# Optimization experiments

Hardware: AMD Instinct MI355X
Metric: run time of the kernel (lower is better)

The kernel has to match this reference:

```python
import jax, jax.numpy as jnp
import numpy as np

EMBED_DIM = 768
NUM_HEADS = 12
HEAD_DIM = EMBED_DIM // NUM_HEADS  # 64
SCALE = HEAD_DIM ** -0.5
B, S = 32, 512


def setup_inputs() -> dict:
    key = jax.random.key(0)
    ks = jax.random.split(key, 10)
    std = EMBED_DIM ** -0.5
    hidden_states = jax.random.normal(ks[0], (B, S, EMBED_DIM), dtype=jnp.float32)
    # causal mask: 0 on/below diagonal, large negative above
    neg = jnp.full((S, S), -1e9, dtype=jnp.float32)
    causal_attention_mask = jnp.broadcast_to(
        jnp.triu(neg, k=1)[None, None, :, :], (B, 1, S, S)
    ).astype(jnp.float32)
    Wq = jax.random.normal(ks[1], (EMBED_DIM, EMBED_DIM), dtype=jnp.float32) * std
    bq = jnp.zeros((EMBED_DIM,), dtype=jnp.float32)
    Wk = jax.random.normal(ks[2], (EMBED_DIM, EMBED_DIM), dtype=jnp.float32) * std
    bk = jnp.zeros((EMBED_DIM,), dtype=jnp.float32)
    Wv = jax.random.normal(ks[3], (EMBED_DIM, EMBED_DIM), dtype=jnp.float32) * std
    bv = jnp.zeros((EMBED_DIM,), dtype=jnp.float32)
    Wo = jax.random.normal(ks[4], (EMBED_DIM, EMBED_DIM), dtype=jnp.float32) * std
    bo = jnp.zeros((EMBED_DIM,), dtype=jnp.float32)
    return {
        "hidden_states": hidden_states,
        "causal_attention_mask": causal_attention_mask,
        "Wq": Wq, "bq": bq, "Wk": Wk, "bk": bk,
        "Wv": Wv, "bv": bv, "Wo": Wo, "bo": bo,
    }


def reference(hidden_states, causal_attention_mask, Wq, bq, Wk, bk, Wv, bv, Wo, bo):
    b, s, e = hidden_states.shape
    # projections; query scaled as in original
    q = (hidden_states @ Wq + bq) * SCALE          # [b,s,e]
    k = hidden_states @ Wk + bk
    v = hidden_states @ Wv + bv
    # [b,h,s,d]
    q = q.reshape(b, s, NUM_HEADS, HEAD_DIM).transpose(0, 2, 1, 3)
    k = k.reshape(b, s, NUM_HEADS, HEAD_DIM).transpose(0, 2, 1, 3)
    v = v.reshape(b, s, NUM_HEADS, HEAD_DIM).transpose(0, 2, 1, 3)
    scores = jnp.einsum("bhqd,bhkd->bhqk", q, k) + causal_attention_mask
    attn = jax.nn.softmax(scores, axis=-1)
    out = jnp.einsum("bhqk,bhkd->bhqd", attn, v)   # [b,h,s,d]
    out = out.transpose(0, 2, 1, 3).reshape(b, s, e)
    return out @ Wo + bo
```

## Files before the change

### kernel.cpp

```cpp
#include <hip/hip_runtime.h>
#include <hip/hip_bf16.h>

typedef __attribute__((ext_vector_type(8))) short bf16x8;
typedef __attribute__((ext_vector_type(4))) float f32x4;
typedef unsigned short u16;
typedef unsigned int u32;

#define MFMA16(a,b,c) __builtin_amdgcn_mfma_f32_16x16x32_bf16((a),(b),(c),0,0,0)
#define FENCE() asm volatile("" ::: "memory")
#define BARRIER() do { FENCE(); __builtin_amdgcn_s_barrier(); FENCE(); } while (0)
#define WAITV(N) asm volatile("s_waitcnt vmcnt(" #N ")" ::: "memory")

__device__ __forceinline__ u16 f2bf(float f) {
  union { float f; u32 u; } c; c.f = f;
  u32 u = c.u;
  return (u16)((u + 0x7FFFu + ((u >> 16) & 1u)) >> 16);
}

__device__ __forceinline__ u32 pk2(float lo, float hi) {
  __hip_bfloat162 h2 = __float22bfloat162_rn(float2{lo, hi});
  union { __hip_bfloat162 h; u32 u; } c; c.h = h2; return c.u;
}

__device__ __forceinline__ void gl_lds16(const u16* g, u16* l) {
  __builtin_amdgcn_global_load_lds((const __attribute__((address_space(1))) void*)g,
                                   (__attribute__((address_space(3))) void*)l, 16, 0, 0);
}

__global__ __launch_bounds__(256) void prep(const float* __restrict__ X,
                                            u16* __restrict__ Xb,
                                            const float* __restrict__ Wq,
                                            const float* __restrict__ Wk,
                                            const float* __restrict__ Wv,
                                            const float* __restrict__ Wo,
                                            u16* __restrict__ WT) {
  const int blk = blockIdx.x, tid = threadIdx.x;
  if (blk < 6144) {
    int i = (blk * 256 + tid) * 8;
    const float4* p = (const float4*)(X + i);
    float4 a = p[0], b = p[1];
    union { u16 h[8]; uint4 v; } o;
    o.h[0] = f2bf(a.x); o.h[1] = f2bf(a.y); o.h[2] = f2bf(a.z); o.h[3] = f2bf(a.w);
    o.h[4] = f2bf(b.x); o.h[5] = f2bf(b.y); o.h[6] = f2bf(b.z); o.h[7] = f2bf(b.w);
    *(uint4*)(Xb + i) = o.v;
  } else {
    __shared__ float t[32][33];
    const int q = blk - 6144;
    const int w = q / 576, p = q % 576;
    const float* W = (w == 0) ? Wq : (w == 1) ? Wk : (w == 2) ? Wv : Wo;
    u16* D = WT + (size_t)w * 768 * 768;
    const int n0 = (p % 24) * 32, k0 = (p / 24) * 32;
    const int tx = tid & 31, ty = tid >> 5;
#pragma unroll
    for (int i = 0; i < 4; ++i)
      t[ty + i * 8][tx] = W[(size_t)(k0 + ty + i * 8) * 768 + n0 + tx];
    __syncthreads();
#pragma unroll
    for (int i = 0; i < 4; ++i)
      D[(size_t)(n0 + ty + i * 8) * 768 + k0 + tx] = f2bf(t[tx][ty + i * 8]);
  }
}


#define STA(bu, t) do { _Pragma("unroll") for (int s_ = 0; s_ < 2; ++s_) { \
    const int r_ = s_ * 128 + srow; \
    gl_lds16(A + (size_t)(M0 + r_) * 768 + (t) * 64 + ((sg ^ (r_ & 7)) << 3), \
             &As[bu][r_ * 64 + sg * 8]); } } while (0)
#define STB(bu, t) do { \
    gl_lds16(BT + (size_t)(N0 + srow) * 768 + (t) * 64 + ((sg ^ (srow & 7)) << 3), \
             &Bs[bu][srow * 64 + sg * 8]); \
    if (srow < 64) { const int r_ = 128 + srow; \
      gl_lds16(BT + (size_t)(N0 + r_) * 768 + (t) * 64 + ((sg ^ (r_ & 7)) << 3), \
               &Bs[bu][r_ * 64 + sg * 8]); } } while (0)

template <int MODE>
__global__ __launch_bounds__(1024, 4)
void gemmN(const u16* __restrict__ A, const u16* __restrict__ BT,
           const float* __restrict__ b0, const float* __restrict__ b1,
           const float* __restrict__ b2,
           u16* __restrict__ oQ, u16* __restrict__ oK, u16* __restrict__ oV,
           float* __restrict__ oF, int nN) {
  constexpr int NT = 12;
  __shared__ __align__(16) u16 As[2][256 * 64];
  __shared__ __align__(16) u16 Bs[2][192 * 64];
  const int tid = threadIdx.x;
  const int wave = tid >> 6, lane = tid & 63;
  const int lg = lane >> 4, l15 = lane & 15;
  const int wr = wave >> 2, wc = wave & 3;
  const int bi = blockIdx.x;
  const int j = bi >> 3;
  const int M0 = ((bi & 7) * 8 + j / nN) * 256;
  const int N0 = (j % nN) * 192;
  const int srow = tid >> 3, sg = tid & 7;

  f32x4 acc[4][3] = {};

  STA(0, 0); STB(0, 0);

#pragma unroll
  for (int t = 0; t < NT; ++t) {
    WAITV(0);
    BARRIER();
    if (t + 1 < NT) { STA((t + 1) & 1, t + 1); STB((t + 1) & 1, t + 1); }
    const int bb = t & 1;
    __builtin_amdgcn_s_setprio(1);
    bf16x8 bfr[3][2];
#pragma unroll
    for (int nt = 0; nt < 3; ++nt)
#pragma unroll
      for (int kh = 0; kh < 2; ++kh) {
        const int row = wc * 48 + nt * 16 + l15;
        bfr[nt][kh] = *(const bf16x8*)&Bs[bb][row * 64 + (((kh * 4 + lg) ^ (row & 7)) << 3)];
      }
#pragma unroll
    for (int mt = 0; mt < 4; ++mt) {
      bf16x8 af[2];
#pragma unroll
      for (int kh = 0; kh < 2; ++kh) {
        const int row = wr * 64 + mt * 16 + l15;
        af[kh] = *(const bf16x8*)&As[bb][row * 64 + (((kh * 4 + lg) ^ (row & 7)) << 3)];
      }
#pragma unroll
      for (int nt = 0; nt < 3; ++nt)
#pragma unroll
        for (int kh = 0; kh < 2; ++kh)
          acc[mt][nt] = MFMA16(af[kh], bfr[nt][kh], acc[mt][nt]);
    }
    __builtin_amdgcn_s_setprio(0);
  }

#pragma unroll
  for (int mt = 0; mt < 4; ++mt) {
    const int r0 = M0 + wr * 64 + mt * 16 + lg * 4;
#pragma unroll
    for (int nt = 0; nt < 3; ++nt) {
      const int ng = N0 + wc * 48 + nt * 16 + l15;
      f32x4 v = acc[mt][nt];
      if (MODE == 1) {
        const float bb = b0[ng];
#pragma unroll
        for (int r = 0; r < 4; ++r)
          oF[(size_t)(r0 + r) * 768 + ng] = v[r] + bb;
      } else {
        const int mat = ng / 768;
        const int col = ng - mat * 768;
        const float bb = (mat == 0 ? b0 : (mat == 1 ? b1 : b2))[col];
        if (mat == 0) {
#pragma unroll
          for (int r = 0; r < 4; ++r)
            oQ[(size_t)(r0 + r) * 768 + col] = f2bf((v[r] + bb) * 0.125f);
        } else if (mat == 1) {
#pragma unroll
          for (int r = 0; r < 4; ++r)
            oK[(size_t)(r0 + r) * 768 + col] = f2bf(v[r] + bb);
        } else {
          const int hh = col >> 6, dd = col & 63;
#pragma unroll
          for (int r = 0; r < 4; ++r) {
            const int rr = r0 + r;
            const int bbx = rr >> 9, ss = rr & 511;
            oV[((size_t)(bbx * 12 + hh) * 64 + dd) * 512 + ss] = f2bf(v[r] + bb);
          }
        }
      }
    }
  }
}

#define STG(bu, kt) do { \
    gl_lds16(Kg0 + (size_t)((kt) * 64 + srow) * 768 + sgr * 8, \
             &Ks[bu][srow * 64 + (tid & 7) * 8]); \
    gl_lds16(Vg0 + (size_t)srow * 512 + (kt) * 64 + sgr * 8, \
             &Vs[bu][srow * 64 + (tid & 7) * 8]); \
  } while (0)

__global__ __launch_bounds__(512, 2)
void flash(const u16* __restrict__ Q, const u16* __restrict__ K,
           const u16* __restrict__ V, u16* __restrict__ O) {
  __shared__ __align__(16) u16 Ks[3][4096];
  __shared__ __align__(16) u16 Vs[3][4096];
  __shared__ __align__(16) u32 Ps[8][16 * 36];
  const int id = blockIdx.x;
  const int qt = id / 384, hb = id % 384;
  const int h = hb % 12, b = hb / 12;
  const int tid = threadIdx.x, wave = tid >> 6, lane = tid & 63;
  const int lg = lane >> 4, l15 = lane & 15;
  const int NT = 2 * qt + 2;
  const int srow = tid >> 3, sgr = (tid & 7) ^ (srow & 7);
  const int qbase = qt * 128 + wave * 16;

  bf16x8 qf[2];
  {
    const u16* qp = Q + (size_t)(b * 512 + qbase + l15) * 768 + h * 64 + lg * 8;
    qf[0] = *(const bf16x8*)qp;
    qf[1] = *(const bf16x8*)(qp + 32);
  }
  f32x4 oacc[4] = {};
  float m_run = -1e30f, l_run = 0.f;
  const u16* Kg0 = K + (size_t)(b * 512) * 768 + h * 64;
  const u16* Vg0 = V + (size_t)(b * 12 + h) * 64 * 512;
  u32* pw = Ps[wave];

  STG(0, 0);
  STG(1, 1);
  for (int kt = 0; kt < NT; ++kt) {
    if (kt < NT - 1) { WAITV(2); } else { WAITV(0); }
    BARRIER();
    if (kt + 2 < NT) STG((kt + 2) % 3, kt + 2);
    const int bu = kt % 3;
    if (kt * 64 <= qbase + 15) {
      f32x4 sc[4] = {};
#pragma unroll
      for (int kc = 0; kc < 2; ++kc)
#pragma unroll
        for (int t = 0; t < 4; ++t) {
          const int row = t * 16 + l15;
          bf16x8 kf = *(const bf16x8*)&Ks[bu][row * 64 + (((kc * 4 + lg) ^ (l15 & 7)) << 3)];
          sc[t] = MFMA16(kf, qf[kc], sc[t]);
        }
      if (kt * 64 + 63 > qbase) {
#pragma unroll
        for (int t = 0; t < 4; ++t)
#pragma unroll
          for (int r = 0; r < 4; ++r)
            if (kt * 64 + t * 16 + lg * 4 + r > qbase + l15) sc[t][r] = -1e30f;
      }
      float pm = sc[0][0];
#pragma unroll
      for (int t = 0; t < 4; ++t)
#pragma unroll
        for (int r = 0; r < 4; ++r) pm = fmaxf(pm, sc[t][r]);
      pm = fmaxf(pm, __shfl_xor(pm, 16));
      pm = fmaxf(pm, __shfl_xor(pm, 32));
      if (__any(pm > m_run + 8.f)) {
        const float mn = fmaxf(m_run, pm);
        const float fs = __expf(m_run - mn);
        m_run = mn;
        l_run *= fs;
#pragma unroll
        for (int t = 0; t < 4; ++t)
#pragma unroll
          for (int r = 0; r < 4; ++r) oacc[t][r] *= fs;
      }
      float rs = 0.f;
#pragma unroll
      for (int t = 0; t < 4; ++t) {
        float p0 = __expf(sc[t][0] - m_run), p1 = __expf(sc[t][1] - m_run);
        float p2 = __expf(sc[t][2] - m_run), p3 = __expf(sc[t][3] - m_run);
        rs += (p0 + p1) + (p2 + p3);
        pw[l15 * 36 + t * 8 + lg * 2 + 0] = pk2(p0, p1);
        pw[l15 * 36 + t * 8 + lg * 2 + 1] = pk2(p2, p3);
      }
      rs += __shfl_xor(rs, 16);
      rs += __shfl_xor(rs, 32);
      l_run += rs;
#pragma unroll
      for (int kc = 0; kc < 2; ++kc) {
        bf16x8 pf = *(const bf16x8*)&pw[l15 * 36 + kc * 16 + lg * 4];
#pragma unroll
        for (int t = 0; t < 4; ++t) {
          const int row = t * 16 + l15;
          bf16x8 vf = *(const bf16x8*)&Vs[bu][row * 64 + (((kc * 4 + lg) ^ (l15 & 7)) << 3)];
          oacc[t] = MFMA16(vf, pf, oacc[t]);
        }
      }
    }
  }
  const float inv = 1.f / l_run;
  u16* op = O + (size_t)(b * 512 + qbase + l15) * 768 + h * 64;
#pragma unroll
  for (int t = 0; t < 4; ++t) {
    uint2 w;
    w.x = pk2(oacc[t][0] * inv, oacc[t][1] * inv);
    w.y = pk2(oacc[t][2] * inv, oacc[t][3] * inv);
    *(uint2*)(op + t * 16 + lg * 4) = w;
  }
}

extern "C" void kernel_launch(void* const* d_in, const int* in_sizes, int n_in,
                              void* d_out, int out_size, void* d_ws, size_t ws_size,
                              hipStream_t stream) {
  (void)in_sizes; (void)n_in; (void)out_size; (void)ws_size;
  const float* X  = (const float*)d_in[0];
  const float* Wq = (const float*)d_in[2];
  const float* bq = (const float*)d_in[3];
  const float* Wk = (const float*)d_in[4];
  const float* bk = (const float*)d_in[5];
  const float* Wv = (const float*)d_in[6];
  const float* bv = (const float*)d_in[7];
  const float* Wo = (const float*)d_in[8];
  const float* bo = (const float*)d_in[9];
  float* out = (float*)d_out;

  const size_t NME = (size_t)16384 * 768;
  u16* Xb  = (u16*)d_ws;
  u16* Qs  = Xb + NME;
  u16* Kb  = Qs + NME;
  u16* Vt  = Kb + NME;
  u16* WT  = Vt + NME;
  u16* WoT = WT + (size_t)2304 * 768;
  u16* Ao  = Xb;

  prep<<<8448, 256, 0, stream>>>(X, Xb, Wq, Wk, Wv, Wo, WT);
  gemmN<0><<<768, 1024, 0, stream>>>(Xb, WT, bq, bk, bv, Qs, Kb, Vt, nullptr, 12);
  flash<<<1536, 512, 0, stream>>>(Qs, Kb, Vt, Ao);
  gemmN<1><<<256, 1024, 0, stream>>>(Ao, WoT, bo, nullptr, nullptr,
                                     nullptr, nullptr, nullptr, out, 4);
}
```

Baseline: 148.2 us.

## Restructure projection GEMM to 8 waves with interleaved staged loads and MFMA

The projection GEMM drops from 16 waves per block to 8, so each wave now computes a 64x96 tile with 24 accumulators instead of 64x48. Each k-step is split into four quarter-phases, and each phase interleaves its LDS fragment reads, part of the next tile's global-to-LDS prefetch, and one MFMA batch, separated by barriers and lgkmcnt waits. The aim is better overlap of memory traffic with matrix work, and more reuse of each fragment across MFMAs. The cost is higher register pressure per wave, many more barriers per iteration, and lower wave-level parallelism.

New measurement: 158.6 us. +7.0%, slower.

```diff
diff --git a/kernel.cpp b/kernel.cpp
--- a/kernel.cpp
+++ b/kernel.cpp
@@ -10,6 +10,8 @@
 #define FENCE() asm volatile("" ::: "memory")
 #define BARRIER() do { FENCE(); __builtin_amdgcn_s_barrier(); FENCE(); } while (0)
 #define WAITV(N) asm volatile("s_waitcnt vmcnt(" #N ")" ::: "memory")
+#define LG0() do { asm volatile("s_waitcnt lgkmcnt(0)" ::: "memory"); \
+                   __builtin_amdgcn_sched_barrier(0); } while (0)
 
 __device__ __forceinline__ u16 f2bf(float f) {
   union { float f; u32 u; } c; c.f = f;
@@ -62,20 +64,31 @@
 }
 
 
-#define STA(bu, t) do { _Pragma("unroll") for (int s_ = 0; s_ < 2; ++s_) { \
-    const int r_ = s_ * 128 + srow; \
-    gl_lds16(A + (size_t)(M0 + r_) * 768 + (t) * 64 + ((sg ^ (r_ & 7)) << 3), \
-             &As[bu][r_ * 64 + sg * 8]); } } while (0)
-#define STB(bu, t) do { \
-    gl_lds16(BT + (size_t)(N0 + srow) * 768 + (t) * 64 + ((sg ^ (srow & 7)) << 3), \
-             &Bs[bu][srow * 64 + sg * 8]); \
-    if (srow < 64) { const int r_ = 128 + srow; \
-      gl_lds16(BT + (size_t)(N0 + r_) * 768 + (t) * 64 + ((sg ^ (r_ & 7)) << 3), \
-               &Bs[bu][r_ * 64 + sg * 8]); } } while (0)
+#define STA4(bu, t, q) do { \
+    const int r_ = (q) * 64 + (tid >> 3); \
+    const int g_ = tid & 7; \
+    gl_lds16(A + (size_t)(M0 + r_) * 768 + (t) * 64 + ((g_ ^ (r_ & 7)) << 3), \
+             &As[bu][r_ * 64 + g_ * 8]); \
+  } while (0)
+#define STBT(bu, t, h) do { \
+    const int r_ = (h) * 64 + (tid >> 3); \
+    const int g_ = tid & 7; \
+    gl_lds16(BT + (size_t)(N0 + r_) * 768 + (t) * 64 + ((g_ ^ (r_ & 7)) << 3), \
+             &Bs[bu][r_ * 64 + g_ * 8]); \
+  } while (0)
+#define RDA(bb, kh) do { _Pragma("unroll") for (int mt_ = 0; mt_ < 4; ++mt_) { \
+    const int row_ = wr * 64 + mt_ * 16 + l15; \
+    af[mt_] = *(const bf16x8*)&As[bb][row_ * 64 + ((((kh) * 4 + lg) ^ (row_ & 7)) << 3)]; } } while (0)
+#define RDB(bb, nh, kh) do { _Pragma("unroll") for (int nt_ = 0; nt_ < 3; ++nt_) { \
+    const int row_ = wc * 96 + (nh) * 48 + nt_ * 16 + l15; \
+    bfr[nt_] = *(const bf16x8*)&Bs[bb][row_ * 64 + ((((kh) * 4 + lg) ^ (row_ & 7)) << 3)]; } } while (0)
+#define MM(nh) do { _Pragma("unroll") for (int mt_ = 0; mt_ < 4; ++mt_) \
+    _Pragma("unroll") for (int nt_ = 0; nt_ < 3; ++nt_) \
+      acc[mt_][(nh) * 3 + nt_] = MFMA16(af[mt_], bfr[nt_], acc[mt_][(nh) * 3 + nt_]); } while (0)
 
 template <int MODE>
-__global__ __launch_bounds__(1024, 4)
-void gemmN(const u16* __restrict__ A, const u16* __restrict__ BT,
+__global__ __launch_bounds__(512)
+void gemmQ(const u16* __restrict__ A, const u16* __restrict__ BT,
            const float* __restrict__ b0, const float* __restrict__ b1,
            const float* __restrict__ b2,
            u16* __restrict__ oQ, u16* __restrict__ oK, u16* __restrict__ oV,
@@ -86,56 +99,52 @@
   const int tid = threadIdx.x;
   const int wave = tid >> 6, lane = tid & 63;
   const int lg = lane >> 4, l15 = lane & 15;
-  const int wr = wave >> 2, wc = wave & 3;
+  const int wr = wave >> 1, wc = wave & 1;
   const int bi = blockIdx.x;
   const int j = bi >> 3;
   const int M0 = ((bi & 7) * 8 + j / nN) * 256;
   const int N0 = (j % nN) * 192;
-  const int srow = tid >> 3, sg = tid & 7;
-
-  f32x4 acc[4][3] = {};
-
-  STA(0, 0); STB(0, 0);
+
+  f32x4 acc[4][6] = {};
+  bf16x8 af[4], bfr[3];
+
+  STA4(0, 0, 0); STA4(0, 0, 1); STA4(0, 0, 2); STA4(0, 0, 3);
+  STBT(0, 0, 0); STBT(0, 0, 1); STBT(0, 0, 2);
+  WAITV(0);
+  BARRIER();
 
 #pragma unroll
   for (int t = 0; t < NT; ++t) {
+    const int bb = t & 1, nb = bb ^ 1;
+    RDA(bb, 0); RDB(bb, 0, 0);
+    if (t + 1 < NT) { STA4(nb, t + 1, 0); STA4(nb, t + 1, 1); STBT(nb, t + 1, 0); }
+    BARRIER(); LG0();
+    __builtin_amdgcn_s_setprio(1); MM(0); __builtin_amdgcn_s_setprio(0);
+    BARRIER();
+    RDB(bb, 1, 0);
+    if (t + 1 < NT) { STA4(nb, t + 1, 2); STBT(nb, t + 1, 1); }
+    BARRIER(); LG0();
+    __builtin_amdgcn_s_setprio(1); MM(1); __builtin_amdgcn_s_setprio(0);
+    BARRIER();
+    RDA(bb, 1); RDB(bb, 0, 1);
+    if (t + 1 < NT) { STA4(nb, t + 1, 3); STBT(nb, t + 1, 2); }
+    BARRIER(); LG0();
+    __builtin_amdgcn_s_setprio(1); MM(0); __builtin_amdgcn_s_setprio(0);
+    BARRIER();
+    RDB(bb, 1, 1);
+    BARRIER(); LG0();
+    __builtin_amdgcn_s_setprio(1); MM(1); __builtin_amdgcn_s_setprio(0);
     WAITV(0);
     BARRIER();
-    if (t + 1 < NT) { STA((t + 1) & 1, t + 1); STB((t + 1) & 1, t + 1); }
-    const int bb = t & 1;
-    __builtin_amdgcn_s_setprio(1);
-    bf16x8 bfr[3][2];
-#pragma unroll
-    for (int nt = 0; nt < 3; ++nt)
-#pragma unroll
-      for (int kh = 0; kh < 2; ++kh) {
-        const int row = wc * 48 + nt * 16 + l15;
-        bfr[nt][kh] = *(const bf16x8*)&Bs[bb][row * 64 + (((kh * 4 + lg) ^ (row & 7)) << 3)];
-      }
-#pragma unroll
-    for (int mt = 0; mt < 4; ++mt) {
-      bf16x8 af[2];
-#pragma unroll
-      for (int kh = 0; kh < 2; ++kh) {
-        const int row = wr * 64 + mt * 16 + l15;
-        af[kh] = *(const bf16x8*)&As[bb][row * 64 + (((kh * 4 + lg) ^ (row & 7)) << 3)];
-      }
-#pragma unroll
-      for (int nt = 0; nt < 3; ++nt)
-#pragma unroll
-        for (int kh = 0; kh < 2; ++kh)
-          acc[mt][nt] = MFMA16(af[kh], bfr[nt][kh], acc[mt][nt]);
-    }
-    __builtin_amdgcn_s_setprio(0);
   }
 
 #pragma unroll
   for (int mt = 0; mt < 4; ++mt) {
     const int r0 = M0 + wr * 64 + mt * 16 + lg * 4;
 #pragma unroll
-    for (int nt = 0; nt < 3; ++nt) {
-      const int ng = N0 + wc * 48 + nt * 16 + l15;
-      f32x4 v = acc[mt][nt];
+    for (int ni = 0; ni < 6; ++ni) {
+      const int ng = N0 + wc * 96 + ni * 16 + l15;
+      f32x4 v = acc[mt][ni];
       if (MODE == 1) {
         const float bb = b0[ng];
 #pragma unroll
@@ -302,8 +311,8 @@
   u16* Ao  = Xb;
 
   prep<<<8448, 256, 0, stream>>>(X, Xb, Wq, Wk, Wv, Wo, WT);
-  gemmN<0><<<768, 1024, 0, stream>>>(Xb, WT, bq, bk, bv, Qs, Kb, Vt, nullptr, 12);
+  gemmQ<0><<<768, 512, 0, stream>>>(Xb, WT, bq, bk, bv, Qs, Kb, Vt, nullptr, 12);
   flash<<<1536, 512, 0, stream>>>(Qs, Kb, Vt, Ao);
-  gemmN<1><<<256, 1024, 0, stream>>>(Ao, WoT, bo, nullptr, nullptr,
-                                     nullptr, nullptr, nullptr, out, 4);
-}
+  gemmQ<1><<<256, 512, 0, stream>>>(Ao, WoT, bo, nullptr, nullptr,
+                                    nullptr, nullptr, nullptr, out, 4);
+}
```
